# Kernel optimization log

Measured on AMD Instinct MI355X. Metric: run time of the kernel, lower is better.

Reference implementation:

```python
import jax, jax.numpy as jnp
import numpy as np

H = 32          # phasor harmonics
DELTA0 = 7.0    # base phasor frequency
HID = 128       # hidden_dim
NEXP = 4        # num_experts
EDIM = 64       # expert_dim
NCLS = 3        # num_classes
IN_DIM = 28 * 28
ENH_DIM = HID + 2 * H  # 192


def setup_inputs() -> dict:
    key = jax.random.key(0)
    ks = jax.random.split(key, 12)
    B = 65536
    s = lambda d: 1.0 / np.sqrt(d)
    return {
        "x": jax.random.normal(ks[0], (B, 28, 28), dtype=jnp.float32),
        "W_in": jax.random.normal(ks[1], (IN_DIM, HID), dtype=jnp.float32) * s(IN_DIM),
        "b_in": jnp.zeros((HID,), dtype=jnp.float32),
        "W_gate": jax.random.normal(ks[2], (ENH_DIM, NEXP), dtype=jnp.float32) * s(ENH_DIM),
        "b_gate": jnp.zeros((NEXP,), dtype=jnp.float32),
        "W_exp": jax.random.normal(ks[3], (NEXP, ENH_DIM, EDIM), dtype=jnp.float32) * s(ENH_DIM),
        "b_exp": jnp.zeros((NEXP, EDIM), dtype=jnp.float32),
        "W_ctx": jax.random.normal(ks[4], (EDIM, HID), dtype=jnp.float32) * s(EDIM),
        "b_ctx": jnp.zeros((HID,), dtype=jnp.float32),
        "W_out": jax.random.normal(ks[5], (HID, NCLS), dtype=jnp.float32) * s(HID),
        "b_out": jnp.zeros((NCLS,), dtype=jnp.float32),
    }


def _phasor_bank(t):
    # t: [B] scalar drive per sample -> [B, 2H] cos/sin harmonic features
    freqs = DELTA0 * jnp.arange(1, H + 1, dtype=t.dtype)  # [H]
    phase = t[:, None] * freqs[None, :]                   # [B, H]
    return jnp.concatenate([jnp.cos(phase), jnp.sin(phase)], axis=-1)


def reference(x, W_in, b_in, W_gate, b_gate, W_exp, b_exp, W_ctx, b_ctx, W_out, b_out):
    B = x.shape[0]
    x_flat = x.reshape((B, -1))                                  # [B, 784]
    projected = x_flat @ W_in + b_in                             # [B, HID]
    t = jnp.mean(projected, axis=-1)                             # [B]
    temporal = _phasor_bank(t)                                   # [B, 2H]
    enhanced = jnp.concatenate([projected, temporal], axis=-1)   # [B, ENH_DIM]
    # Expert retrieval core: softmax gate over NEXP experts
    gate = jax.nn.softmax(enhanced @ W_gate + b_gate, axis=-1)   # [B, NEXP]
    expert_out = jax.nn.relu(
        jnp.einsum('bd,edh->beh', enhanced, W_exp) + b_exp[None] # [B, NEXP, EDIM]
    )
    combined = jnp.einsum('be,beh->bh', gate, expert_out)        # [B, EDIM]
    context = jnp.tanh(combined @ W_ctx + b_ctx)                 # [B, HID]
    logits = context @ W_out + b_out                             # [B, NCLS]
    return logits
```

## Files before the change

### kernel.cpp

```cpp
#include <hip/hip_runtime.h>

typedef unsigned short u16;
typedef unsigned int u32;
typedef __attribute__((ext_vector_type(8))) short short8;
typedef __attribute__((ext_vector_type(4))) float f32x4;

#define OFF_WM    0
#define OFF_WINF  3584
#define OFF_WEGF  208384
#define OFF_WCTXF 312832
#define OFF_WOUTF 329216

__device__ __forceinline__ u16 f2bf(float x) {
  union { float f; u32 u; } v; v.f = x;
  u32 r = v.u + 0x7FFFu + ((v.u >> 16) & 1u);
  return (u16)(r >> 16);
}

__global__ void prep_kernel(const float* __restrict__ W_in, const float* __restrict__ b_in,
                            const float* __restrict__ W_gate, const float* __restrict__ W_exp,
                            const float* __restrict__ W_ctx, const float* __restrict__ W_out,
                            float* __restrict__ wm, u16* __restrict__ WinF,
                            u16* __restrict__ WegF, u16* __restrict__ WctxF,
                            u16* __restrict__ WoutF) {
  int idx = blockIdx.x * 256 + threadIdx.x;
  if (idx < 801) {
    if (idx == 800) {
      float s = 0.f;
      for (int j = 0; j < 128; ++j) s += b_in[j];
      wm[800] = s * (1.f / 128.f);
    } else if (idx >= 784) {
      wm[idx] = 0.f;
    } else {
      float s = 0.f;
      for (int j = 0; j < 128; ++j) s += W_in[idx * 128 + j];
      wm[idx] = s * (1.f / 128.f);
    }
  } else if (idx < 103201) {
    int f = idx - 801;
    int j = f & 7, lane = (f >> 3) & 63, tile = f >> 9;
    int ct = tile & 7, kt = tile >> 3;
    int k = kt * 32 + ((lane >> 4) << 3) + j;
    int n = ct * 16 + (lane & 15);
    WinF[f] = (k < 784) ? f2bf(W_in[k * 128 + n]) : (u16)0;
  } else if (idx < 155425) {
    int f = idx - 103201;
    int j = f & 7, lane = (f >> 3) & 63, tile = f >> 9;
    int kt = tile / 17, ct = tile - kt * 17;
    int k = kt * 32 + ((lane >> 4) << 3) + j;
    int n = ct * 16 + (lane & 15);
    float v = 0.f;
    if (n < 256) { int e = n >> 6, h = n & 63; v = W_exp[(e * 192 + k) * 64 + h]; }
    else if (n < 260) v = W_gate[k * 4 + (n - 256)];
    WegF[f] = f2bf(v);
  } else if (idx < 163617) {
    int f = idx - 155425;
    int j = f & 7, lane = (f >> 3) & 63, tile = f >> 9;
    int ct = tile & 7, kt = tile >> 3;
    int k = kt * 32 + ((lane >> 4) << 3) + j;
    int n = ct * 16 + (lane & 15);
    WctxF[f] = f2bf(W_ctx[k * 128 + n]);
  } else if (idx < 165665) {
    int f = idx - 163617;
    int j = f & 7, lane = (f >> 3) & 63, kt = f >> 9;
    int k = kt * 32 + ((lane >> 4) << 3) + j;
    int n = lane & 15;
    WoutF[f] = (n < 3) ? f2bf(W_out[k * 3 + n]) : (u16)0;
  }
}

__global__ __launch_bounds__(256, 2)
void fused_kernel(const float* __restrict__ x,
                  const float* __restrict__ b_in, const float* __restrict__ b_gate,
                  const float* __restrict__ b_exp, const float* __restrict__ b_ctx,
                  const float* __restrict__ b_out,
                  const float* __restrict__ wm, const u16* __restrict__ WinF,
                  const u16* __restrict__ WegF, const u16* __restrict__ WctxF,
                  const u16* __restrict__ WoutF,
                  float* __restrict__ out) {
  __shared__ __align__(16) u16 smem[4 * 7680];
  const int tid = threadIdx.x;
  const int wv = tid >> 6;
  const int ln = tid & 63;
  const int cb = ln & 15;
  const int qr = ln >> 4;
  u16* enh0 = smem + wv * 7680;
  u16* enh1 = enh0 + 3840;
  u16* cmb0 = enh0;
  u16* cmb1 = enh1;
  u16* ctx0 = enh0 + 1280;
  u16* ctx1 = enh1 + 1280;

  const int grow = blockIdx.x * 128 + wv * 32;
  const float* xr0 = x + (size_t)(grow + cb) * 784;
  const float* xr1 = xr0 + (size_t)16 * 784;

  const f32x4 vz = {0.f, 0.f, 0.f, 0.f};

  f32x4 acc0[8], acc1[8];
  #pragma unroll
  for (int i = 0; i < 8; ++i) { acc0[i] = vz; acc1[i] = vz; }
  float tp0 = 0.f, tp1 = 0.f;

  const u16* wbase = WinF + ln * 8;
  for (int kt = 0; kt < 25; ++kt) {
    const u16* wb = wbase + (size_t)kt * 4096;
    short8 Bf[8];
    #pragma unroll
    for (int ct = 0; ct < 8; ++ct)
      Bf[ct] = *(const short8*)(wb + ct * 512);

    const int k0 = kt * 32 + qr * 8;
    float4 a0 = make_float4(0.f, 0.f, 0.f, 0.f), a1 = a0;
    float4 b0 = a0, b1 = a0, m0 = a0, m1 = a0;
    if (k0 < 784) {
      a0 = *(const float4*)(xr0 + k0);
      a1 = *(const float4*)(xr0 + k0 + 4);
      b0 = *(const float4*)(xr1 + k0);
      b1 = *(const float4*)(xr1 + k0 + 4);
      m0 = *(const float4*)(wm + k0);
      m1 = *(const float4*)(wm + k0 + 4);
      tp0 += a0.x * m0.x + a0.y * m0.y + a0.z * m0.z + a0.w * m0.w
           + a1.x * m1.x + a1.y * m1.y + a1.z * m1.z + a1.w * m1.w;
      tp1 += b0.x * m0.x + b0.y * m0.y + b0.z * m0.z + b0.w * m0.w
           + b1.x * m1.x + b1.y * m1.y + b1.z * m1.z + b1.w * m1.w;
    }
    union { short8 s; u32 u[4]; } af, bf;
    af.u[0] = (u32)f2bf(a0.x) | ((u32)f2bf(a0.y) << 16);
    af.u[1] = (u32)f2bf(a0.z) | ((u32)f2bf(a0.w) << 16);
    af.u[2] = (u32)f2bf(a1.x) | ((u32)f2bf(a1.y) << 16);
    af.u[3] = (u32)f2bf(a1.z) | ((u32)f2bf(a1.w) << 16);
    bf.u[0] = (u32)f2bf(b0.x) | ((u32)f2bf(b0.y) << 16);
    bf.u[1] = (u32)f2bf(b0.z) | ((u32)f2bf(b0.w) << 16);
    bf.u[2] = (u32)f2bf(b1.x) | ((u32)f2bf(b1.y) << 16);
    bf.u[3] = (u32)f2bf(b1.z) | ((u32)f2bf(b1.w) << 16);

    #pragma unroll
    for (int ct = 0; ct < 8; ++ct) {
      acc0[ct] = __builtin_amdgcn_mfma_f32_16x16x32_bf16(af.s, Bf[ct], acc0[ct], 0, 0, 0);
      acc1[ct] = __builtin_amdgcn_mfma_f32_16x16x32_bf16(bf.s, Bf[ct], acc1[ct], 0, 0, 0);
    }
  }

  tp0 += __shfl_xor(tp0, 16);
  tp0 += __shfl_xor(tp0, 32);
  tp1 += __shfl_xor(tp1, 16);
  tp1 += __shfl_xor(tp1, 32);
  const float mb = wm[800];
  const float t0 = tp0 + mb;
  const float t1 = tp1 + mb;

  #pragma unroll
  for (int ct = 0; ct < 8; ++ct) {
    float bi = b_in[ct * 16 + cb];
    u16* d0 = enh0 + (ct >> 1) * 640 + (ct & 1) * 16 + cb;
    u16* d1 = enh1 + (ct >> 1) * 640 + (ct & 1) * 16 + cb;
    #pragma unroll
    for (int i = 0; i < 4; ++i) {
      d0[(qr * 4 + i) * 40] = f2bf(acc0[ct][i] + bi);
      d1[(qr * 4 + i) * 40] = f2bf(acc1[ct][i] + bi);
    }
  }
  #pragma unroll
  for (int g = 0; g < 2; ++g) {
    float t = g ? t1 : t0;
    u16* eW = g ? enh1 : enh0;
    float phi = 7.f * t;
    float ss, cc, sd, cd;
    sincosf(phi * (float)(qr * 8 + 1), &ss, &cc);
    sincosf(phi, &sd, &cd);
    u16* pc = eW + 4 * 640 + cb * 40 + qr * 8;
    u16* ps = eW + 5 * 640 + cb * 40 + qr * 8;
    #pragma unroll
    for (int m = 0; m < 8; ++m) {
      pc[m] = f2bf(cc);
      ps[m] = f2bf(ss);
      float nc = cc * cd - ss * sd;
      ss = ss * cd + cc * sd;
      cc = nc;
    }
  }

  const u16* gbase = WegF + ln * 8;
  f32x4 g0 = vz, g1 = vz;
  #pragma unroll
  for (int kt = 0; kt < 6; ++kt) {
    short8 A0 = *(const short8*)(enh0 + kt * 640 + cb * 40 + qr * 8);
    short8 A1 = *(const short8*)(enh1 + kt * 640 + cb * 40 + qr * 8);
    short8 Bg = *(const short8*)(gbase + (size_t)(kt * 17 + 16) * 512);
    g0 = __builtin_amdgcn_mfma_f32_16x16x32_bf16(A0, Bg, g0, 0, 0, 0);
    g1 = __builtin_amdgcn_mfma_f32_16x16x32_bf16(A1, Bg, g1, 0, 0, 0);
  }

  float ge0[4][4], ge1[4][4];
  {
    float bg = b_gate[cb & 3];
    #pragma unroll
    for (int i = 0; i < 4; ++i) {
      {
        float gi = g0[i] + bg;
        float mx = fmaxf(gi, __shfl_xor(gi, 1));
        mx = fmaxf(mx, __shfl_xor(mx, 2));
        float ev = __expf(gi - mx);
        float sv = ev + __shfl_xor(ev, 1);
        sv += __shfl_xor(sv, 2);
        float g = ev / sv;
        int base = qr * 16;
        ge0[0][i] = __shfl(g, base + 0);
        ge0[1][i] = __shfl(g, base + 1);
        ge0[2][i] = __shfl(g, base + 2);
        ge0[3][i] = __shfl(g, base + 3);
      }
      {
        float gi = g1[i] + bg;
        float mx = fmaxf(gi, __shfl_xor(gi, 1));
        mx = fmaxf(mx, __shfl_xor(mx, 2));
        float ev = __expf(gi - mx);
        float sv = ev + __shfl_xor(ev, 1);
        sv += __shfl_xor(sv, 2);
        float g = ev / sv;
        int base = qr * 16;
        ge1[0][i] = __shfl(g, base + 0);
        ge1[1][i] = __shfl(g, base + 1);
        ge1[2][i] = __shfl(g, base + 2);
        ge1[3][i] = __shfl(g, base + 3);
      }
    }
  }

  f32x4 cA[4], cB[4];
  #pragma unroll
  for (int i = 0; i < 4; ++i) { cA[i] = vz; cB[i] = vz; }
  #pragma unroll
  for (int e = 0; e < 4; ++e) {
    f32x4 ae0[4], ae1[4];
    #pragma unroll
    for (int i = 0; i < 4; ++i) { ae0[i] = vz; ae1[i] = vz; }
    #pragma unroll
    for (int kt = 0; kt < 6; ++kt) {
      short8 A0 = *(const short8*)(enh0 + kt * 640 + cb * 40 + qr * 8);
      short8 A1 = *(const short8*)(enh1 + kt * 640 + cb * 40 + qr * 8);
      const u16* gb = gbase + (size_t)(kt * 17 + e * 4) * 512;
      #pragma unroll
      for (int c2 = 0; c2 < 4; ++c2) {
        short8 Bf = *(const short8*)(gb + c2 * 512);
        ae0[c2] = __builtin_amdgcn_mfma_f32_16x16x32_bf16(A0, Bf, ae0[c2], 0, 0, 0);
        ae1[c2] = __builtin_amdgcn_mfma_f32_16x16x32_bf16(A1, Bf, ae1[c2], 0, 0, 0);
      }
    }
    #pragma unroll
    for (int c2 = 0; c2 < 4; ++c2) {
      float be = b_exp[e * 64 + c2 * 16 + cb];
      #pragma unroll
      for (int i = 0; i < 4; ++i) {
        cA[c2][i] += ge0[e][i] * fmaxf(ae0[c2][i] + be, 0.f);
        cB[c2][i] += ge1[e][i] * fmaxf(ae1[c2][i] + be, 0.f);
      }
    }
  }
  #pragma unroll
  for (int c2 = 0; c2 < 4; ++c2) {
    u16* d0 = cmb0 + (c2 >> 1) * 640 + (c2 & 1) * 16 + cb;
    u16* d1 = cmb1 + (c2 >> 1) * 640 + (c2 & 1) * 16 + cb;
    #pragma unroll
    for (int i = 0; i < 4; ++i) {
      d0[(qr * 4 + i) * 40] = f2bf(cA[c2][i]);
      d1[(qr * 4 + i) * 40] = f2bf(cB[c2][i]);
    }
  }

  f32x4 c30[8], c31[8];
  #pragma unroll
  for (int i = 0; i < 8; ++i) { c30[i] = vz; c31[i] = vz; }
  #pragma unroll
  for (int kt = 0; kt < 2; ++kt) {
    short8 A0 = *(const short8*)(cmb0 + kt * 640 + cb * 40 + qr * 8);
    short8 A1 = *(const short8*)(cmb1 + kt * 640 + cb * 40 + qr * 8);
    #pragma unroll
    for (int ct = 0; ct < 8; ++ct) {
      short8 Bf = *(const short8*)(WctxF + ((kt * 8 + ct) * 64 + ln) * 8);
      c30[ct] = __builtin_amdgcn_mfma_f32_16x16x32_bf16(A0, Bf, c30[ct], 0, 0, 0);
      c31[ct] = __builtin_amdgcn_mfma_f32_16x16x32_bf16(A1, Bf, c31[ct], 0, 0, 0);
    }
  }
  #pragma unroll
  for (int ct = 0; ct < 8; ++ct) {
    float bc = b_ctx[ct * 16 + cb];
    u16* d0 = ctx0 + ct * 16 + cb;
    u16* d1 = ctx1 + ct * 16 + cb;
    #pragma unroll
    for (int i = 0; i < 4; ++i) {
      float v0 = c30[ct][i] + bc;
      float e0 = __expf(2.f * v0);
      d0[(qr * 4 + i) * 136] = f2bf(1.f - 2.f / (e0 + 1.f));
      float v1 = c31[ct][i] + bc;
      float e1 = __expf(2.f * v1);
      d1[(qr * 4 + i) * 136] = f2bf(1.f - 2.f / (e1 + 1.f));
    }
  }

  f32x4 a40 = vz, a41 = vz;
  #pragma unroll
  for (int kt = 0; kt < 4; ++kt) {
    short8 A0 = *(const short8*)(ctx0 + cb * 136 + kt * 32 + qr * 8);
    short8 A1 = *(const short8*)(ctx1 + cb * 136 + kt * 32 + qr * 8);
    short8 Bf = *(const short8*)(WoutF + (kt * 64 + ln) * 8);
    a40 = __builtin_amdgcn_mfma_f32_16x16x32_bf16(A0, Bf, a40, 0, 0, 0);
    a41 = __builtin_amdgcn_mfma_f32_16x16x32_bf16(A1, Bf, a41, 0, 0, 0);
  }
  if (cb < 3) {
    float bo = b_out[cb];
    #pragma unroll
    for (int i = 0; i < 4; ++i) {
      out[(size_t)(grow + qr * 4 + i) * 3 + cb] = a40[i] + bo;
      out[(size_t)(grow + 16 + qr * 4 + i) * 3 + cb] = a41[i] + bo;
    }
  }
}

extern "C" void kernel_launch(void* const* d_in, const int* in_sizes, int n_in,
                              void* d_out, int out_size, void* d_ws, size_t ws_size,
                              hipStream_t stream) {
  const float* x      = (const float*)d_in[0];
  const float* W_in   = (const float*)d_in[1];
  const float* b_in   = (const float*)d_in[2];
  const float* W_gate = (const float*)d_in[3];
  const float* b_gate = (const float*)d_in[4];
  const float* W_exp  = (const float*)d_in[5];
  const float* b_exp  = (const float*)d_in[6];
  const float* W_ctx  = (const float*)d_in[7];
  const float* b_ctx  = (const float*)d_in[8];
  const float* W_out  = (const float*)d_in[9];
  const float* b_out  = (const float*)d_in[10];
  float* out = (float*)d_out;

  char* ws = (char*)d_ws;
  float* wm  = (float*)(ws + OFF_WM);
  u16* WinF  = (u16*)(ws + OFF_WINF);
  u16* WegF  = (u16*)(ws + OFF_WEGF);
  u16* WctxF = (u16*)(ws + OFF_WCTXF);
  u16* WoutF = (u16*)(ws + OFF_WOUTF);

  const int B = in_sizes[0] / 784;
  prep_kernel<<<648, 256, 0, stream>>>(W_in, b_in, W_gate, W_exp, W_ctx, W_out,
                                       wm, WinF, WegF, WctxF, WoutF);
  fused_kernel<<<B / 128, 256, 0, stream>>>(x, b_in, b_gate, b_exp, b_ctx, b_out,
                                            wm, WinF, WegF, WctxF, WoutF, out);
}
```

Baseline: 339.5 us.

## Process four 16-row groups per wave to reuse weight fragments

Each wave now computes 64 rows instead of 32, so every W_in/expert/ctx weight fragment loaded from global feeds twice as many MFMAs. Block size covers 256 rows, the grid halves, and LDS per block doubles. Launch bounds drop to one block per CU, trading occupancy and latency hiding for less weight traffic per row.

```diff
diff --git a/kernel.cpp b/kernel.cpp
--- a/kernel.cpp
+++ b/kernel.cpp
@@ -69,7 +69,7 @@
   }
 }
 
-__global__ __launch_bounds__(256, 2)
+__global__ __launch_bounds__(256, 1)
 void fused_kernel(const float* __restrict__ x,
                   const float* __restrict__ b_in, const float* __restrict__ b_gate,
                   const float* __restrict__ b_exp, const float* __restrict__ b_ctx,
@@ -78,29 +78,30 @@
                   const u16* __restrict__ WegF, const u16* __restrict__ WctxF,
                   const u16* __restrict__ WoutF,
                   float* __restrict__ out) {
-  __shared__ __align__(16) u16 smem[4 * 7680];
+  __shared__ __align__(16) u16 smem[4 * 15360];
   const int tid = threadIdx.x;
   const int wv = tid >> 6;
   const int ln = tid & 63;
   const int cb = ln & 15;
   const int qr = ln >> 4;
-  u16* enh0 = smem + wv * 7680;
-  u16* enh1 = enh0 + 3840;
-  u16* cmb0 = enh0;
-  u16* cmb1 = enh1;
-  u16* ctx0 = enh0 + 1280;
-  u16* ctx1 = enh1 + 1280;
-
-  const int grow = blockIdx.x * 128 + wv * 32;
-  const float* xr0 = x + (size_t)(grow + cb) * 784;
-  const float* xr1 = xr0 + (size_t)16 * 784;
+
+  u16* eh[4];
+  #pragma unroll
+  for (int g = 0; g < 4; ++g) eh[g] = smem + wv * 15360 + g * 3840;
+
+  const int grow = blockIdx.x * 256 + wv * 64;
+  const float* xrs[4];
+  #pragma unroll
+  for (int g = 0; g < 4; ++g) xrs[g] = x + (size_t)(grow + g * 16 + cb) * 784;
 
   const f32x4 vz = {0.f, 0.f, 0.f, 0.f};
 
-  f32x4 acc0[8], acc1[8];
-  #pragma unroll
-  for (int i = 0; i < 8; ++i) { acc0[i] = vz; acc1[i] = vz; }
-  float tp0 = 0.f, tp1 = 0.f;
+  f32x4 acc[4][8];
+  #pragma unroll
+  for (int g = 0; g < 4; ++g)
+    #pragma unroll
+    for (int i = 0; i < 8; ++i) acc[g][i] = vz;
+  float tp[4] = {0.f, 0.f, 0.f, 0.f};
 
   const u16* wbase = WinF + ln * 8;
   for (int kt = 0; kt < 25; ++kt) {
@@ -111,66 +112,63 @@
       Bf[ct] = *(const short8*)(wb + ct * 512);
 
     const int k0 = kt * 32 + qr * 8;
-    float4 a0 = make_float4(0.f, 0.f, 0.f, 0.f), a1 = a0;
-    float4 b0 = a0, b1 = a0, m0 = a0, m1 = a0;
+    short8 afs[4];
     if (k0 < 784) {
-      a0 = *(const float4*)(xr0 + k0);
-      a1 = *(const float4*)(xr0 + k0 + 4);
-      b0 = *(const float4*)(xr1 + k0);
-      b1 = *(const float4*)(xr1 + k0 + 4);
-      m0 = *(const float4*)(wm + k0);
-      m1 = *(const float4*)(wm + k0 + 4);
-      tp0 += a0.x * m0.x + a0.y * m0.y + a0.z * m0.z + a0.w * m0.w
-           + a1.x * m1.x + a1.y * m1.y + a1.z * m1.z + a1.w * m1.w;
-      tp1 += b0.x * m0.x + b0.y * m0.y + b0.z * m0.z + b0.w * m0.w
-           + b1.x * m1.x + b1.y * m1.y + b1.z * m1.z + b1.w * m1.w;
-    }
-    union { short8 s; u32 u[4]; } af, bf;
-    af.u[0] = (u32)f2bf(a0.x) | ((u32)f2bf(a0.y) << 16);
-    af.u[1] = (u32)f2bf(a0.z) | ((u32)f2bf(a0.w) << 16);
-    af.u[2] = (u32)f2bf(a1.x) | ((u32)f2bf(a1.y) << 16);
-    af.u[3] = (u32)f2bf(a1.z) | ((u32)f2bf(a1.w) << 16);
-    bf.u[0] = (u32)f2bf(b0.x) | ((u32)f2bf(b0.y) << 16);
-    bf.u[1] = (u32)f2bf(b0.z) | ((u32)f2bf(b0.w) << 16);
-    bf.u[2] = (u32)f2bf(b1.x) | ((u32)f2bf(b1.y) << 16);
-    bf.u[3] = (u32)f2bf(b1.z) | ((u32)f2bf(b1.w) << 16);
+      const float4 m0 = *(const float4*)(wm + k0);
+      const float4 m1 = *(const float4*)(wm + k0 + 4);
+      #pragma unroll
+      for (int g = 0; g < 4; ++g) {
+        float4 a0 = *(const float4*)(xrs[g] + k0);
+        float4 a1 = *(const float4*)(xrs[g] + k0 + 4);
+        tp[g] += a0.x * m0.x + a0.y * m0.y + a0.z * m0.z + a0.w * m0.w
+               + a1.x * m1.x + a1.y * m1.y + a1.z * m1.z + a1.w * m1.w;
+        union { short8 s; u32 u[4]; } af;
+        af.u[0] = (u32)f2bf(a0.x) | ((u32)f2bf(a0.y) << 16);
+        af.u[1] = (u32)f2bf(a0.z) | ((u32)f2bf(a0.w) << 16);
+        af.u[2] = (u32)f2bf(a1.x) | ((u32)f2bf(a1.y) << 16);
+        af.u[3] = (u32)f2bf(a1.z) | ((u32)f2bf(a1.w) << 16);
+        afs[g] = af.s;
+      }
+    } else {
+      #pragma unroll
+      for (int g = 0; g < 4; ++g) afs[g] = short8{0,0,0,0,0,0,0,0};
+    }
 
     #pragma unroll
     for (int ct = 0; ct < 8; ++ct) {
-      acc0[ct] = __builtin_amdgcn_mfma_f32_16x16x32_bf16(af.s, Bf[ct], acc0[ct], 0, 0, 0);
-      acc1[ct] = __builtin_amdgcn_mfma_f32_16x16x32_bf16(bf.s, Bf[ct], acc1[ct], 0, 0, 0);
-    }
-  }
-
-  tp0 += __shfl_xor(tp0, 16);
-  tp0 += __shfl_xor(tp0, 32);
-  tp1 += __shfl_xor(tp1, 16);
-  tp1 += __shfl_xor(tp1, 32);
+      #pragma unroll
+      for (int g = 0; g < 4; ++g)
+        acc[g][ct] = __builtin_amdgcn_mfma_f32_16x16x32_bf16(afs[g], Bf[ct], acc[g][ct], 0, 0, 0);
+    }
+  }
+
+  #pragma unroll
+  for (int g = 0; g < 4; ++g) {
+    tp[g] += __shfl_xor(tp[g], 16);
+    tp[g] += __shfl_xor(tp[g], 32);
+  }
   const float mb = wm[800];
-  const float t0 = tp0 + mb;
-  const float t1 = tp1 + mb;
 
   #pragma unroll
   for (int ct = 0; ct < 8; ++ct) {
     float bi = b_in[ct * 16 + cb];
-    u16* d0 = enh0 + (ct >> 1) * 640 + (ct & 1) * 16 + cb;
-    u16* d1 = enh1 + (ct >> 1) * 640 + (ct & 1) * 16 + cb;
-    #pragma unroll
-    for (int i = 0; i < 4; ++i) {
-      d0[(qr * 4 + i) * 40] = f2bf(acc0[ct][i] + bi);
-      d1[(qr * 4 + i) * 40] = f2bf(acc1[ct][i] + bi);
-    }
-  }
-  #pragma unroll
-  for (int g = 0; g < 2; ++g) {
-    float t = g ? t1 : t0;
-    u16* eW = g ? enh1 : enh0;
+    #pragma unroll
+    for (int g = 0; g < 4; ++g) {
+      u16* dst = eh[g] + (ct >> 1) * 640 + (ct & 1) * 16 + cb;
+      #pragma unroll
+      for (int i = 0; i < 4; ++i)
+        dst[(qr * 4 + i) * 40] = f2bf(acc[g][ct][i] + bi);
+    }
+  }
+  #pragma unroll
+  for (int g = 0; g < 4; ++g) {
+    float t = tp[g] + mb;
     float phi = 7.f * t;
     float ss, cc, sd, cd;
     sincosf(phi * (float)(qr * 8 + 1), &ss, &cc);
     sincosf(phi, &sd, &cd);
-    u16* pc = eW + 4 * 640 + cb * 40 + qr * 8;
-    u16* ps = eW + 5 * 640 + cb * 40 + qr * 8;
+    u16* pc = eh[g] + 4 * 640 + cb * 40 + qr * 8;
+    u16* ps = eh[g] + 5 * 640 + cb * 40 + qr * 8;
     #pragma unroll
     for (int m = 0; m < 8; ++m) {
       pc[m] = f2bf(cc);
@@ -182,139 +180,153 @@
   }
 
   const u16* gbase = WegF + ln * 8;
-  f32x4 g0 = vz, g1 = vz;
-  #pragma unroll
-  for (int kt = 0; kt < 6; ++kt) {
-    short8 A0 = *(const short8*)(enh0 + kt * 640 + cb * 40 + qr * 8);
-    short8 A1 = *(const short8*)(enh1 + kt * 640 + cb * 40 + qr * 8);
-    short8 Bg = *(const short8*)(gbase + (size_t)(kt * 17 + 16) * 512);
-    g0 = __builtin_amdgcn_mfma_f32_16x16x32_bf16(A0, Bg, g0, 0, 0, 0);
-    g1 = __builtin_amdgcn_mfma_f32_16x16x32_bf16(A1, Bg, g1, 0, 0, 0);
-  }
-
-  float ge0[4][4], ge1[4][4];
-  {
-    float bg = b_gate[cb & 3];
-    #pragma unroll
-    for (int i = 0; i < 4; ++i) {
-      {
-        float gi = g0[i] + bg;
-        float mx = fmaxf(gi, __shfl_xor(gi, 1));
-        mx = fmaxf(mx, __shfl_xor(mx, 2));
-        float ev = __expf(gi - mx);
-        float sv = ev + __shfl_xor(ev, 1);
-        sv += __shfl_xor(sv, 2);
-        float g = ev / sv;
-        int base = qr * 16;
-        ge0[0][i] = __shfl(g, base + 0);
-        ge0[1][i] = __shfl(g, base + 1);
-        ge0[2][i] = __shfl(g, base + 2);
-        ge0[3][i] = __shfl(g, base + 3);
-      }
-      {
-        float gi = g1[i] + bg;
-        float mx = fmaxf(gi, __shfl_xor(gi, 1));
-        mx = fmaxf(mx, __shfl_xor(mx, 2));
-        float ev = __expf(gi - mx);
-        float sv = ev + __shfl_xor(ev, 1);
-        sv += __shfl_xor(sv, 2);
-        float g = ev / sv;
-        int base = qr * 16;
-        ge1[0][i] = __shfl(g, base + 0);
-        ge1[1][i] = __shfl(g, base + 1);
-        ge1[2][i] = __shfl(g, base + 2);
-        ge1[3][i] = __shfl(g, base + 3);
-      }
-    }
-  }
-
-  f32x4 cA[4], cB[4];
-  #pragma unroll
-  for (int i = 0; i < 4; ++i) { cA[i] = vz; cB[i] = vz; }
-  #pragma unroll
-  for (int e = 0; e < 4; ++e) {
-    f32x4 ae0[4], ae1[4];
-    #pragma unroll
-    for (int i = 0; i < 4; ++i) { ae0[i] = vz; ae1[i] = vz; }
+  #pragma unroll
+  for (int p = 0; p < 2; ++p) {
+    u16* e0 = eh[2 * p];
+    u16* e1 = eh[2 * p + 1];
+
+    f32x4 g0 = vz, g1 = vz;
     #pragma unroll
     for (int kt = 0; kt < 6; ++kt) {
-      short8 A0 = *(const short8*)(enh0 + kt * 640 + cb * 40 + qr * 8);
-      short8 A1 = *(const short8*)(enh1 + kt * 640 + cb * 40 + qr * 8);
-      const u16* gb = gbase + (size_t)(kt * 17 + e * 4) * 512;
+      short8 A0 = *(const short8*)(e0 + kt * 640 + cb * 40 + qr * 8);
+      short8 A1 = *(const short8*)(e1 + kt * 640 + cb * 40 + qr * 8);
+      short8 Bg = *(const short8*)(gbase + (size_t)(kt * 17 + 16) * 512);
+      g0 = __builtin_amdgcn_mfma_f32_16x16x32_bf16(A0, Bg, g0, 0, 0, 0);
+      g1 = __builtin_amdgcn_mfma_f32_16x16x32_bf16(A1, Bg, g1, 0, 0, 0);
+    }
+
+    float ge0[4][4], ge1[4][4];
+    {
+      float bg = b_gate[cb & 3];
+      #pragma unroll
+      for (int i = 0; i < 4; ++i) {
+        {
+          float gi = g0[i] + bg;
+          float mx = fmaxf(gi, __shfl_xor(gi, 1));
+          mx = fmaxf(mx, __shfl_xor(mx, 2));
+          float ev = __expf(gi - mx);
+          float sv = ev + __shfl_xor(ev, 1);
+          sv += __shfl_xor(sv, 2);
+          float g = ev / sv;
+          int base = qr * 16;
+          ge0[0][i] = __shfl(g, base + 0);
+          ge0[1][i] = __shfl(g, base + 1);
+          ge0[2][i] = __shfl(g, base + 2);
+          ge0[3][i] = __shfl(g, base + 3);
+        }
+        {
+          float gi = g1[i] + bg;
+          float mx = fmaxf(gi, __shfl_xor(gi, 1));
+          mx = fmaxf(mx, __shfl_xor(mx, 2));
+          float ev = __expf(gi - mx);
+          float sv = ev + __shfl_xor(ev, 1);
+          sv += __shfl_xor(sv, 2);
+          float g = ev / sv;
+          int base = qr * 16;
+          ge1[0][i] = __shfl(g, base + 0);
+          ge1[1][i] = __shfl(g, base + 1);
+          ge1[2][i] = __shfl(g, base + 2);
+          ge1[3][i] = __shfl(g, base + 3);
+        }
+      }
+    }
+
+    f32x4 cA[4], cB[4];
+    #pragma unroll
+    for (int i = 0; i < 4; ++i) { cA[i] = vz; cB[i] = vz; }
+    #pragma unroll
+    for (int e = 0; e < 4; ++e) {
+      f32x4 ae0[4], ae1[4];
+      #pragma unroll
+      for (int i = 0; i < 4; ++i) { ae0[i] = vz; ae1[i] = vz; }
+      #pragma unroll
+      for (int kt = 0; kt < 6; ++kt) {
+        short8 A0 = *(const short8*)(e0 + kt * 640 + cb * 40 + qr * 8);
+        short8 A1 = *(const short8*)(e1 + kt * 640 + cb * 40 + qr * 8);
+        const u16* gb = gbase + (size_t)(kt * 17 + e * 4) * 512;
+        #pragma unroll
+        for (int c2 = 0; c2 < 4; ++c2) {
+          short8 Bf = *(const short8*)(gb + c2 * 512);
+          ae0[c2] = __builtin_amdgcn_mfma_f32_16x16x32_bf16(A0, Bf, ae0[c2], 0, 0, 0);
+          ae1[c2] = __builtin_amdgcn_mfma_f32_16x16x32_bf16(A1, Bf, ae1[c2], 0, 0, 0);
+        }
+      }
       #pragma unroll
       for (int c2 = 0; c2 < 4; ++c2) {
-        short8 Bf = *(const short8*)(gb + c2 * 512);
-        ae0[c2] = __builtin_amdgcn_mfma_f32_16x16x32_bf16(A0, Bf, ae0[c2], 0, 0, 0);
-        ae1[c2] = __builtin_amdgcn_mfma_f32_16x16x32_bf16(A1, Bf, ae1[c2], 0, 0, 0);
+        float be = b_exp[e * 64 + c2 * 16 + cb];
+        #pragma unroll
+        for (int i = 0; i < 4; ++i) {
+          cA[c2][i] += ge0[e][i] * fmaxf(ae0[c2][i] + be, 0.f);
+          cB[c2][i] += ge1[e][i] * fmaxf(ae1[c2][i] + be, 0.f);
+        }
       }
     }
     #pragma unroll
     for (int c2 = 0; c2 < 4; ++c2) {
-      float be = b_exp[e * 64 + c2 * 16 + cb];
+      u16* d0 = e0 + (c2 >> 1) * 640 + (c2 & 1) * 16 + cb;
+      u16* d1 = e1 + (c2 >> 1) * 640 + (c2 & 1) * 16 + cb;
       #pragma unroll
       for (int i = 0; i < 4; ++i) {
-        cA[c2][i] += ge0[e][i] * fmaxf(ae0[c2][i] + be, 0.f);
-        cB[c2][i] += ge1[e][i] * fmaxf(ae1[c2][i] + be, 0.f);
-      }
-    }
-  }
-  #pragma unroll
-  for (int c2 = 0; c2 < 4; ++c2) {
-    u16* d0 = cmb0 + (c2 >> 1) * 640 + (c2 & 1) * 16 + cb;
-    u16* d1 = cmb1 + (c2 >> 1) * 640 + (c2 & 1) * 16 + cb;
-    #pragma unroll
-    for (int i = 0; i < 4; ++i) {
-      d0[(qr * 4 + i) * 40] = f2bf(cA[c2][i]);
-      d1[(qr * 4 + i) * 40] = f2bf(cB[c2][i]);
-    }
-  }
-
-  f32x4 c30[8], c31[8];
-  #pragma unroll
-  for (int i = 0; i < 8; ++i) { c30[i] = vz; c31[i] = vz; }
-  #pragma unroll
-  for (int kt = 0; kt < 2; ++kt) {
-    short8 A0 = *(const short8*)(cmb0 + kt * 640 + cb * 40 + qr * 8);
-    short8 A1 = *(const short8*)(cmb1 + kt * 640 + cb * 40 + qr * 8);
+        d0[(qr * 4 + i) * 40] = f2bf(cA[c2][i]);
+        d1[(qr * 4 + i) * 40] = f2bf(cB[c2][i]);
+      }
+    }
+  }
+
+  #pragma unroll
+  for (int p = 0; p < 2; ++p) {
+    u16* e0 = eh[2 * p];
+    u16* e1 = eh[2 * p + 1];
+    f32x4 c30[8], c31[8];
+    #pragma unroll
+    for (int i = 0; i < 8; ++i) { c30[i] = vz; c31[i] = vz; }
+    #pragma unroll
+    for (int kt = 0; kt < 2; ++kt) {
+      short8 A0 = *(const short8*)(e0 + kt * 640 + cb * 40 + qr * 8);
+      short8 A1 = *(const short8*)(e1 + kt * 640 + cb * 40 + qr * 8);
+      #pragma unroll
+      for (int ct = 0; ct < 8; ++ct) {
+        short8 Bf = *(const short8*)(WctxF + ((kt * 8 + ct) * 64 + ln) * 8);
+        c30[ct] = __builtin_amdgcn_mfma_f32_16x16x32_bf16(A0, Bf, c30[ct], 0, 0, 0);
+        c31[ct] = __builtin_amdgcn_mfma_f32_16x16x32_bf16(A1, Bf, c31[ct], 0, 0, 0);
+      }
+    }
     #pragma unroll
     for (int ct = 0; ct < 8; ++ct) {
-      short8 Bf = *(const short8*)(WctxF + ((kt * 8 + ct) * 64 + ln) * 8);
-      c30[ct] = __builtin_amdgcn_mfma_f32_16x16x32_bf16(A0, Bf, c30[ct], 0, 0, 0);
-      c31[ct] = __builtin_amdgcn_mfma_f32_16x16x32_bf16(A1, Bf, c31[ct], 0, 0, 0);
-    }
-  }
-  #pragma unroll
-  for (int ct = 0; ct < 8; ++ct) {
-    float bc = b_ctx[ct * 16 + cb];
-    u16* d0 = ctx0 + ct * 16 + cb;
-    u16* d1 = ctx1 + ct * 16 + cb;
-    #pragma unroll
-    for (int i = 0; i < 4; ++i) {
-      float v0 = c30[ct][i] + bc;
-      float e0 = __expf(2.f * v0);
-      d0[(qr * 4 + i) * 136] = f2bf(1.f - 2.f / (e0 + 1.f));
-      float v1 = c31[ct][i] + bc;
-      float e1 = __expf(2.f * v1);
-      d1[(qr * 4 + i) * 136] = f2bf(1.f - 2.f / (e1 + 1.f));
-    }
-  }
-
-  f32x4 a40 = vz, a41 = vz;
+      float bc = b_ctx[ct * 16 + cb];
+      u16* d0 = e0 + 1280 + ct * 16 + cb;
+      u16* d1 = e1 + 1280 + ct * 16 + cb;
+      #pragma unroll
+      for (int i = 0; i < 4; ++i) {
+        float v0 = c30[ct][i] + bc;
+        float x0 = __expf(2.f * v0);
+        d0[(qr * 4 + i) * 136] = f2bf(1.f - 2.f / (x0 + 1.f));
+        float v1 = c31[ct][i] + bc;
+        float x1 = __expf(2.f * v1);
+        d1[(qr * 4 + i) * 136] = f2bf(1.f - 2.f / (x1 + 1.f));
+      }
+    }
+  }
+
+  f32x4 a4[4];
+  #pragma unroll
+  for (int g = 0; g < 4; ++g) a4[g] = vz;
   #pragma unroll
   for (int kt = 0; kt < 4; ++kt) {
-    short8 A0 = *(const short8*)(ctx0 + cb * 136 + kt * 32 + qr * 8);
-    short8 A1 = *(const short8*)(ctx1 + cb * 136 + kt * 32 + qr * 8);
     short8 Bf = *(const short8*)(WoutF + (kt * 64 + ln) * 8);
-    a40 = __builtin_amdgcn_mfma_f32_16x16x32_bf16(A0, Bf, a40, 0, 0, 0);
-    a41 = __builtin_amdgcn_mfma_f32_16x16x32_bf16(A1, Bf, a41, 0, 0, 0);
+    #pragma unroll
+    for (int g = 0; g < 4; ++g) {
+      short8 A = *(const short8*)(eh[g] + 1280 + cb * 136 + kt * 32 + qr * 8);
+      a4[g] = __builtin_amdgcn_mfma_f32_16x16x32_bf16(A, Bf, a4[g], 0, 0, 0);
+    }
   }
   if (cb < 3) {
     float bo = b_out[cb];
     #pragma unroll
-    for (int i = 0; i < 4; ++i) {
-      out[(size_t)(grow + qr * 4 + i) * 3 + cb] = a40[i] + bo;
-      out[(size_t)(grow + 16 + qr * 4 + i) * 3 + cb] = a41[i] + bo;
-    }
+    for (int g = 0; g < 4; ++g)
+      #pragma unroll
+      for (int i = 0; i < 4; ++i)
+        out[(size_t)(grow + g * 16 + qr * 4 + i) * 3 + cb] = a4[g][i] + bo;
   }
 }
 
@@ -344,6 +356,6 @@
   const int B = in_sizes[0] / 784;
   prep_kernel<<<648, 256, 0, stream>>>(W_in, b_in, W_gate, W_exp, W_ctx, W_out,
                                        wm, WinF, WegF, WctxF, WoutF);
-  fused_kernel<<<B / 128, 256, 0, stream>>>(x, b_in, b_gate, b_exp, b_ctx, b_out,
+  fused_kernel<<<B / 256, 256, 0, stream>>>(x, b_in, b_gate, b_exp, b_ctx, b_out,
                                             wm, WinF, WegF, WctxF, WoutF, out);
 }
```

New measurement: 362.5 us. +6.8%, slower.

## Stage weight fragments in shared memory with double-buffered W_in prefetch

Applied to the files above, without the earlier changes.

Weight fragments for the input projection, expert, context and output GEMMs are cooperatively loaded once per block into a shared staging buffer instead of being fetched from global memory by every wave. The input projection loop double-buffers the next k-tile in registers and LDS. The expert GEMM is reordered to iterate k outermost with all expert column tiles accumulated together. This aims to cut redundant L2 traffic, at the cost of more LDS, more registers and many extra block barriers.

```diff
diff --git a/kernel.cpp b/kernel.cpp
--- a/kernel.cpp
+++ b/kernel.cpp
@@ -78,7 +78,7 @@
                   const u16* __restrict__ WegF, const u16* __restrict__ WctxF,
                   const u16* __restrict__ WoutF,
                   float* __restrict__ out) {
-  __shared__ __align__(16) u16 smem[4 * 7680];
+  __shared__ __align__(16) u16 smem[4 * 7680 + 8192];
   const int tid = threadIdx.x;
   const int wv = tid >> 6;
   const int ln = tid & 63;
@@ -90,6 +90,7 @@
   u16* cmb1 = enh1;
   u16* ctx0 = enh0 + 1280;
   u16* ctx1 = enh1 + 1280;
+  u16* stg  = smem + 4 * 7680;
 
   const int grow = blockIdx.x * 128 + wv * 32;
   const float* xr0 = x + (size_t)(grow + cb) * 784;
@@ -102,44 +103,69 @@
   for (int i = 0; i < 8; ++i) { acc0[i] = vz; acc1[i] = vz; }
   float tp0 = 0.f, tp1 = 0.f;
 
-  const u16* wbase = WinF + ln * 8;
+  {
+    const u16* src = WinF + tid * 8;
+    short8 r0 = *(const short8*)(src);
+    short8 r1 = *(const short8*)(src + 2048);
+    *(short8*)(stg + tid * 8) = r0;
+    *(short8*)(stg + 2048 + tid * 8) = r1;
+  }
+  __syncthreads();
+
   for (int kt = 0; kt < 25; ++kt) {
-    const u16* wb = wbase + (size_t)kt * 4096;
+    const int buf = (kt & 1) << 12;
+    short8 r0 = short8{0,0,0,0,0,0,0,0}, r1 = r0;
+    const bool pf = (kt < 24);
+    if (pf) {
+      const u16* src = WinF + (size_t)(kt + 1) * 4096 + tid * 8;
+      r0 = *(const short8*)(src);
+      r1 = *(const short8*)(src + 2048);
+    }
+
+    const int k0 = kt * 32 + qr * 8;
+    union { short8 s; u32 u[4]; } af, bf;
+    {
+      float4 a0 = make_float4(0.f, 0.f, 0.f, 0.f), a1 = a0;
+      float4 b0 = a0, b1 = a0, m0 = a0, m1 = a0;
+      if (k0 < 784) {
+        a0 = *(const float4*)(xr0 + k0);
+        a1 = *(const float4*)(xr0 + k0 + 4);
+        b0 = *(const float4*)(xr1 + k0);
+        b1 = *(const float4*)(xr1 + k0 + 4);
+        m0 = *(const float4*)(wm + k0);
+        m1 = *(const float4*)(wm + k0 + 4);
+        tp0 += a0.x * m0.x + a0.y * m0.y + a0.z * m0.z + a0.w * m0.w
+             + a1.x * m1.x + a1.y * m1.y + a1.z * m1.z + a1.w * m1.w;
+        tp1 += b0.x * m0.x + b0.y * m0.y + b0.z * m0.z + b0.w * m0.w
+             + b1.x * m1.x + b1.y * m1.y + b1.z * m1.z + b1.w * m1.w;
+      }
+      af.u[0] = (u32)f2bf(a0.x) | ((u32)f2bf(a0.y) << 16);
+      af.u[1] = (u32)f2bf(a0.z) | ((u32)f2bf(a0.w) << 16);
+      af.u[2] = (u32)f2bf(a1.x) | ((u32)f2bf(a1.y) << 16);
+      af.u[3] = (u32)f2bf(a1.z) | ((u32)f2bf(a1.w) << 16);
+      bf.u[0] = (u32)f2bf(b0.x) | ((u32)f2bf(b0.y) << 16);
+      bf.u[1] = (u32)f2bf(b0.z) | ((u32)f2bf(b0.w) << 16);
+      bf.u[2] = (u32)f2bf(b1.x) | ((u32)f2bf(b1.y) << 16);
+      bf.u[3] = (u32)f2bf(b1.z) | ((u32)f2bf(b1.w) << 16);
+    }
+
     short8 Bf[8];
     #pragma unroll
     for (int ct = 0; ct < 8; ++ct)
-      Bf[ct] = *(const short8*)(wb + ct * 512);
-
-    const int k0 = kt * 32 + qr * 8;
-    float4 a0 = make_float4(0.f, 0.f, 0.f, 0.f), a1 = a0;
-    float4 b0 = a0, b1 = a0, m0 = a0, m1 = a0;
-    if (k0 < 784) {
-      a0 = *(const float4*)(xr0 + k0);
-      a1 = *(const float4*)(xr0 + k0 + 4);
-      b0 = *(const float4*)(xr1 + k0);
-      b1 = *(const float4*)(xr1 + k0 + 4);
-      m0 = *(const float4*)(wm + k0);
-      m1 = *(const float4*)(wm + k0 + 4);
-      tp0 += a0.x * m0.x + a0.y * m0.y + a0.z * m0.z + a0.w * m0.w
-           + a1.x * m1.x + a1.y * m1.y + a1.z * m1.z + a1.w * m1.w;
-      tp1 += b0.x * m0.x + b0.y * m0.y + b0.z * m0.z + b0.w * m0.w
-           + b1.x * m1.x + b1.y * m1.y + b1.z * m1.z + b1.w * m1.w;
-    }
-    union { short8 s; u32 u[4]; } af, bf;
-    af.u[0] = (u32)f2bf(a0.x) | ((u32)f2bf(a0.y) << 16);
-    af.u[1] = (u32)f2bf(a0.z) | ((u32)f2bf(a0.w) << 16);
-    af.u[2] = (u32)f2bf(a1.x) | ((u32)f2bf(a1.y) << 16);
-    af.u[3] = (u32)f2bf(a1.z) | ((u32)f2bf(a1.w) << 16);
-    bf.u[0] = (u32)f2bf(b0.x) | ((u32)f2bf(b0.y) << 16);
-    bf.u[1] = (u32)f2bf(b0.z) | ((u32)f2bf(b0.w) << 16);
-    bf.u[2] = (u32)f2bf(b1.x) | ((u32)f2bf(b1.y) << 16);
-    bf.u[3] = (u32)f2bf(b1.z) | ((u32)f2bf(b1.w) << 16);
+      Bf[ct] = *(const short8*)(stg + buf + ct * 512 + ln * 8);
 
     #pragma unroll
     for (int ct = 0; ct < 8; ++ct) {
       acc0[ct] = __builtin_amdgcn_mfma_f32_16x16x32_bf16(af.s, Bf[ct], acc0[ct], 0, 0, 0);
       acc1[ct] = __builtin_amdgcn_mfma_f32_16x16x32_bf16(bf.s, Bf[ct], acc1[ct], 0, 0, 0);
     }
+
+    if (pf) {
+      u16* dst = stg + (buf ^ 4096);
+      *(short8*)(dst + tid * 8) = r0;
+      *(short8*)(dst + 2048 + tid * 8) = r1;
+    }
+    __syncthreads();
   }
 
   tp0 += __shfl_xor(tp0, 16);
@@ -228,33 +254,45 @@
     }
   }
 
+  f32x4 ae0[16], ae1[16];
+  #pragma unroll
+  for (int c = 0; c < 16; ++c) { ae0[c] = vz; ae1[c] = vz; }
+  for (int kt = 0; kt < 6; ++kt) {
+    __syncthreads();
+    {
+      const u16* src = WegF + (size_t)kt * 17 * 512 + tid * 8;
+      short8 s0 = *(const short8*)(src);
+      short8 s1 = *(const short8*)(src + 2048);
+      short8 s2 = *(const short8*)(src + 4096);
+      short8 s3 = *(const short8*)(src + 6144);
+      *(short8*)(stg + tid * 8) = s0;
+      *(short8*)(stg + 2048 + tid * 8) = s1;
+      *(short8*)(stg + 4096 + tid * 8) = s2;
+      *(short8*)(stg + 6144 + tid * 8) = s3;
+    }
+    __syncthreads();
+    short8 A0 = *(const short8*)(enh0 + kt * 640 + cb * 40 + qr * 8);
+    short8 A1 = *(const short8*)(enh1 + kt * 640 + cb * 40 + qr * 8);
+    #pragma unroll
+    for (int c = 0; c < 16; ++c) {
+      short8 Bf = *(const short8*)(stg + c * 512 + ln * 8);
+      ae0[c] = __builtin_amdgcn_mfma_f32_16x16x32_bf16(A0, Bf, ae0[c], 0, 0, 0);
+      ae1[c] = __builtin_amdgcn_mfma_f32_16x16x32_bf16(A1, Bf, ae1[c], 0, 0, 0);
+    }
+  }
+
   f32x4 cA[4], cB[4];
   #pragma unroll
   for (int i = 0; i < 4; ++i) { cA[i] = vz; cB[i] = vz; }
   #pragma unroll
   for (int e = 0; e < 4; ++e) {
-    f32x4 ae0[4], ae1[4];
-    #pragma unroll
-    for (int i = 0; i < 4; ++i) { ae0[i] = vz; ae1[i] = vz; }
-    #pragma unroll
-    for (int kt = 0; kt < 6; ++kt) {
-      short8 A0 = *(const short8*)(enh0 + kt * 640 + cb * 40 + qr * 8);
-      short8 A1 = *(const short8*)(enh1 + kt * 640 + cb * 40 + qr * 8);
-      const u16* gb = gbase + (size_t)(kt * 17 + e * 4) * 512;
-      #pragma unroll
-      for (int c2 = 0; c2 < 4; ++c2) {
-        short8 Bf = *(const short8*)(gb + c2 * 512);
-        ae0[c2] = __builtin_amdgcn_mfma_f32_16x16x32_bf16(A0, Bf, ae0[c2], 0, 0, 0);
-        ae1[c2] = __builtin_amdgcn_mfma_f32_16x16x32_bf16(A1, Bf, ae1[c2], 0, 0, 0);
-      }
-    }
     #pragma unroll
     for (int c2 = 0; c2 < 4; ++c2) {
       float be = b_exp[e * 64 + c2 * 16 + cb];
       #pragma unroll
       for (int i = 0; i < 4; ++i) {
-        cA[c2][i] += ge0[e][i] * fmaxf(ae0[c2][i] + be, 0.f);
-        cB[c2][i] += ge1[e][i] * fmaxf(ae1[c2][i] + be, 0.f);
+        cA[c2][i] += ge0[e][i] * fmaxf(ae0[e * 4 + c2][i] + be, 0.f);
+        cB[c2][i] += ge1[e][i] * fmaxf(ae1[e * 4 + c2][i] + be, 0.f);
       }
     }
   }
@@ -269,6 +307,19 @@
     }
   }
 
+  __syncthreads();
+  {
+    const u16* src = WctxF + tid * 8;
+    short8 s0 = *(const short8*)(src);
+    short8 s1 = *(const short8*)(src + 2048);
+    short8 s2 = *(const short8*)(src + 4096);
+    short8 s3 = *(const short8*)(src + 6144);
+    *(short8*)(stg + tid * 8) = s0;
+    *(short8*)(stg + 2048 + tid * 8) = s1;
+    *(short8*)(stg + 4096 + tid * 8) = s2;
+    *(short8*)(stg + 6144 + tid * 8) = s3;
+  }
+  __syncthreads();
   f32x4 c30[8], c31[8];
   #pragma unroll
   for (int i = 0; i < 8; ++i) { c30[i] = vz; c31[i] = vz; }
@@ -278,7 +329,7 @@
     short8 A1 = *(const short8*)(cmb1 + kt * 640 + cb * 40 + qr * 8);
     #pragma unroll
     for (int ct = 0; ct < 8; ++ct) {
-      short8 Bf = *(const short8*)(WctxF + ((kt * 8 + ct) * 64 + ln) * 8);
+      short8 Bf = *(const short8*)(stg + (kt * 8 + ct) * 512 + ln * 8);
       c30[ct] = __builtin_amdgcn_mfma_f32_16x16x32_bf16(A0, Bf, c30[ct], 0, 0, 0);
       c31[ct] = __builtin_amdgcn_mfma_f32_16x16x32_bf16(A1, Bf, c31[ct], 0, 0, 0);
     }
@@ -299,12 +350,18 @@
     }
   }
 
+  __syncthreads();
+  {
+    short8 s0 = *(const short8*)(WoutF + tid * 8);
+    *(short8*)(stg + tid * 8) = s0;
+  }
+  __syncthreads();
   f32x4 a40 = vz, a41 = vz;
   #pragma unroll
   for (int kt = 0; kt < 4; ++kt) {
     short8 A0 = *(const short8*)(ctx0 + cb * 136 + kt * 32 + qr * 8);
     short8 A1 = *(const short8*)(ctx1 + cb * 136 + kt * 32 + qr * 8);
-    short8 Bf = *(const short8*)(WoutF + (kt * 64 + ln) * 8);
+    short8 Bf = *(const short8*)(stg + kt * 512 + ln * 8);
     a40 = __builtin_amdgcn_mfma_f32_16x16x32_bf16(A0, Bf, a40, 0, 0, 0);
     a41 = __builtin_amdgcn_mfma_f32_16x16x32_bf16(A1, Bf, a41, 0, 0, 0);
   }
```

New measurement: 328.1 us (median of 2 runs). -3.4%, faster.
